# Performance work log

Measured on AMD Instinct MI355X. Metric: run time of the kernel, lower is better.

Reference implementation:

```python
import jax, jax.numpy as jnp
from jax import lax
import numpy as np

NS, NQ = 115, 23          # support / query node counts (1 node per graph here)
GS, GQ, C = 115, 23, 23   # support graphs (5-shot x 23-way), query graphs, classes
D = 1024


def _seg_mean(x, idx, n):
    # scatter-mean along axis 0 (matches torch_scatter reduce='mean'; empty segments -> 0)
    s = jax.ops.segment_sum(x, idx, num_segments=n)
    cnt = jax.ops.segment_sum(jnp.ones(x.shape[0], x.dtype), idx, num_segments=n)
    return s / jnp.maximum(cnt, 1.0).reshape((n,) + (1,) * (x.ndim - 1))


def _cnn(x, cw1, cb1, cw_rest, cb_rest):
    def block(h, w, b):
        h = lax.conv_general_dilated(h, w, (1, 1), 'SAME',
                                     dimension_numbers=('NCHW', 'OIHW', 'NCHW'))
        h = jax.nn.relu(h + b[None, :, None, None])
        return lax.reduce_window(h, -jnp.inf, lax.max, (1, 1, 2, 2), (1, 1, 2, 2), 'VALID')
    x = block(x, cw1, cb1)
    for i in range(cw_rest.shape[0]):
        x = block(x, cw_rest[i], cb_rest[i])
    return x.reshape(x.shape[0], -1)  # [N, 1024]


def _agg_mean(x, edge_index, n):
    # PyG propagate: message x_j = x[src], scatter-mean onto dst
    return _seg_mean(x[edge_index[0]], edge_index[1], n)


def setup_inputs() -> dict:
    key = jax.random.key(0)
    ks = jax.random.split(key, 12)
    s = 0.05
    return {
        'support_x': jax.random.normal(ks[0], (NS, 3, 256, 256), jnp.float32),
        'support_edge_index': jax.random.randint(ks[1], (2, 4096), 0, NS),
        'support_batch': jnp.arange(NS),          # 1 node per support graph
        'support_y': jnp.arange(GS) // 5,         # 5 graphs per class, classes 0..22
        'query_x': jax.random.normal(ks[2], (NQ, 3, 256, 256), jnp.float32),
        'query_edge_index': jax.random.randint(ks[3], (2, 1024), 0, NQ),
        'query_batch': jnp.arange(NQ),            # 1 node per query graph
        'query_y': jax.random.randint(ks[4], (GQ,), 0, C),
        'center': jax.random.normal(ks[5], (C, D), jnp.float32),
        'cw1': jax.random.normal(ks[6], (64, 3, 3, 3), jnp.float32) * s,
        'cb1': jnp.zeros((64,), jnp.float32),
        'cw_rest': jax.random.normal(ks[7], (5, 64, 64, 3, 3), jnp.float32) * s,
        'cb_rest': jnp.zeros((5, 64), jnp.float32),
        'lin2_w': jax.random.normal(ks[8], (D, D), jnp.float32) * 0.03,   # [in,out]
        'lin2_b': jnp.zeros((D,), jnp.float32),
        'mlp_w': jax.random.normal(ks[9], (2 * D, D), jnp.float32) * 0.02,  # [in,out]
        'mlp_b': jnp.zeros((D,), jnp.float32),
    }


def reference(support_x, support_edge_index, support_batch, support_y,
              query_x, query_edge_index, query_batch, query_y, center,
              cw1, cb1, cw_rest, cb_rest, lin2_w, lin2_b, mlp_w, mlp_b):
    n_cls = center.shape[0]

    def feats(x, ei):
        n = x.shape[0]
        h1 = _cnn(x, cw1, cb1, cw_rest, cb_rest)          # conv1 s_x1 = x (flatten feats)
        sx = _agg_mean(h1, ei, n) * h1                    # conv1 update: agg * x
        h2 = sx @ lin2_w + lin2_b                         # conv2 Linear(1024,1024)
        h2 = _agg_mean(h2, ei, n) * h2                    # conv2 update: agg * x
        return jnp.concatenate([h1, h2], axis=-1) @ mlp_w + mlp_b  # [N, 1024]

    s_x = feats(support_x, support_edge_index)            # [Ns, D]
    q_x = feats(query_x, query_edge_index)                # [Nq, D]
    gs = support_y.shape[0]
    gq = query_y.shape[0]

    # per-query-node RBF distances, scatter-mean over support graphs, log-softmax over D
    a = jnp.exp(-(s_x[None, :, :] - q_x[:, None, :]) ** 2)        # [Nq, Ns, D]
    a = _seg_mean(jnp.transpose(a, (1, 0, 2)), support_batch, gs) # [Gs, Nq, D]
    pd = jax.nn.log_softmax(jnp.transpose(a, (1, 0, 2)), axis=-1) # [Nq, Gs, D]

    s_xg = _seg_mean(s_x, support_batch, gs)              # [Gs, D]
    q_xg = _seg_mean(q_x, query_batch, gq)                # [Gq, D]
    pd = _seg_mean(pd, query_batch, gq)                   # [Gq, Gs, D]

    s_c = 0.25 * jnp.repeat(center, 5, axis=0) + 0.5 * s_xg       # [Gs, D]
    b = (jnp.exp(-(s_c[None, :, :] - q_xg[:, None, :]) ** 2) + pd).sum(-1)  # [Gq, Gs]
    b = jax.nn.log_softmax(b, axis=-1)
    dis = _seg_mean(b.T, support_y, n_cls).T              # [Gq, C]

    center_new = _seg_mean(s_xg, support_y, n_cls) * 0.5 + 0.25 * center

    y = jax.nn.one_hot(query_y, n_cls, dtype=jnp.float32)
    loss = -(y * jax.nn.log_softmax(dis, axis=-1)).sum()  # F.cross_entropy(soft, sum)
    acc = (jnp.argmax(dis, axis=1) == query_y).astype(jnp.float32).sum()
    return loss, acc, center_new
```

## Files before the change

### kernel.cpp

```cpp
#include <hip/hip_runtime.h>
#include <cstdint>
#include <cstddef>


typedef _Float16 f16x8 __attribute__((ext_vector_type(8)));
typedef __attribute__((ext_vector_type(4))) float f32x4;

#define WL 36864

__global__ __launch_bounds__(256)
void wtransform(const float* __restrict__ cwr, const float* __restrict__ cw1,
                _Float16* __restrict__ wbuf5, _Float16* __restrict__ w1buf) {
  int i = blockIdx.x * 256 + threadIdx.x;
  if (i < 184320) {
    int layer = i / 36864; int rem = i - layer * 36864;
    int tap = rem / 4096;  int r2 = rem - tap * 4096;
    int cc = r2 / 2048;    int r3 = r2 - cc * 2048;
    int nt = r3 / 512;     int r4 = r3 - nt * 512;
    int lane = r4 / 8;     int j = r4 - lane * 8;
    int ic = cc * 32 + (lane >> 4) * 8 + j;
    int oc = nt * 16 + (lane & 15);
    float w = cwr[(((size_t)layer * 64 + oc) * 64 + ic) * 9 + tap];
    wbuf5[(size_t)layer * 36864 + tap * 4096 + (cc * 4 + nt) * 512 + lane * 8 + j] =
        (_Float16)w;
  } else if (i < 184320 + 2048) {
    int e = i - 184320;
    int nt = e / 512; int r4 = e - nt * 512;
    int lane = r4 / 8; int j = r4 - lane * 8;
    int k = (lane >> 4) * 8 + j;
    float w = 0.f;
    if (k < 27) {
      int tap = k / 3, ic = k - tap * 3;
      int oc = nt * 16 + (lane & 15);
      w = cw1[((size_t)oc * 3 + ic) * 9 + tap];
    }
    w1buf[nt * 512 + lane * 8 + j] = (_Float16)w;
  }
}

__global__ __launch_bounds__(256)
void wtransform_lin(const float* __restrict__ w, _Float16* __restrict__ frag,
                    int KS) {
  int i = blockIdx.x * 256 + threadIdx.x;
  int total = KS * 64 * 512;
  if (i >= total) return;
  int ks = i / (64 * 512); int rem = i - ks * (64 * 512);
  int nt = rem / 512;      int r = rem - nt * 512;
  int lane = r / 8;        int j = r - lane * 8;
  int k = ks * 32 + (lane >> 4) * 8 + j;
  int n = nt * 16 + (lane & 15);
  frag[((size_t)ks * 64 + nt) * 512 + lane * 8 + j] = (_Float16)w[(size_t)k * 1024 + n];
}

template<int KTOT>
__global__ __launch_bounds__(256)
void gemm_mfma(const float* __restrict__ A1, const float* __restrict__ A2,
               const _Float16* __restrict__ frag,
               const float* __restrict__ bias, float* __restrict__ out, int M) {
  __shared__ f32x4 s_red[4][2][64];
  const int tid = threadIdx.x;
  const int wave = tid >> 6, lane = tid & 63;
  const int q = lane >> 4, ml = lane & 15;
  const int m0 = blockIdx.y * 16;
  const int nb = blockIdx.x;
  int row = m0 + ml; if (row >= M) row = M - 1;

  f32x4 acc[2];
#pragma unroll
  for (int nt = 0; nt < 2; ++nt) acc[nt] = (f32x4){0.f, 0.f, 0.f, 0.f};

  constexpr int KSW = KTOT / 128;
  const int ksBase = wave * KSW;
#pragma unroll 2
  for (int s = 0; s < KSW; ++s) {
    int ks = ksBase + s;
    int k0 = ks * 32 + q * 8;
    const float* ap;
    if constexpr (KTOT == 2048) {
      ap = (k0 >= 1024) ? (A2 + (size_t)row * 1024 + (k0 - 1024))
                        : (A1 + (size_t)row * 1024 + k0);
    } else {
      ap = A1 + (size_t)row * 1024 + k0;
    }
    float4 va = *(const float4*)ap;
    float4 vb = *(const float4*)(ap + 4);
    f16x8 av;
    av[0] = (_Float16)va.x; av[1] = (_Float16)va.y;
    av[2] = (_Float16)va.z; av[3] = (_Float16)va.w;
    av[4] = (_Float16)vb.x; av[5] = (_Float16)vb.y;
    av[6] = (_Float16)vb.z; av[7] = (_Float16)vb.w;
    const _Float16* fb = frag + ((size_t)ks * 64 + nb * 2) * 512 + lane * 8;
#pragma unroll
    for (int nt = 0; nt < 2; ++nt) {
      f16x8 bv = *(const f16x8*)(fb + nt * 512);
      acc[nt] = __builtin_amdgcn_mfma_f32_16x16x32_f16(av, bv, acc[nt], 0, 0, 0);
    }
  }
#pragma unroll
  for (int nt = 0; nt < 2; ++nt) s_red[wave][nt][lane] = acc[nt];
  __syncthreads();
  if (wave < 2) {
    int nt = wave;
    f32x4 sum = s_red[0][nt][lane];
#pragma unroll
    for (int w2 = 1; w2 < 4; ++w2) {
      f32x4 p = s_red[w2][nt][lane];
      sum[0] += p[0]; sum[1] += p[1]; sum[2] += p[2]; sum[3] += p[3];
    }
    int n = nb * 32 + nt * 16 + ml;
    float bv = bias[n];
#pragma unroll
    for (int r = 0; r < 4; ++r) {
      int m = m0 + q * 4 + r;
      if (m < M) out[(size_t)m * 1024 + n] = sum[r] + bv;
    }
  }
}

template<int TCX, int TCY, bool FP32OUT>
__global__ __launch_bounds__(256, 4)
void conv_mfma(const _Float16* __restrict__ act_in,
               void* __restrict__ act_out,
               const _Float16* __restrict__ wbuf,
               const float* __restrict__ bias,
               int IH, int IW) {
  constexpr int PX = TCX + 2, PY = TCY + 2;
  constexpr int MT = (TCX * TCY) / 64;
  __shared__ __align__(16) _Float16 s_patch[PY * PX * 40];

  const int tid = threadIdx.x;
  const int wave = tid >> 6, lane = tid & 63;
  const int q = lane >> 4, ml = lane & 15;
  const int x0 = blockIdx.x * TCX, y0 = blockIdx.y * TCY;
  const int img = blockIdx.z;

  f32x4 acc[MT][4];
#pragma unroll
  for (int mt = 0; mt < MT; ++mt)
#pragma unroll
    for (int nt = 0; nt < 4; ++nt)
      acc[mt][nt] = (f32x4){0.f, 0.f, 0.f, 0.f};

  int pxv[MT], pyv[MT];
#pragma unroll
  for (int mt = 0; mt < MT; ++mt) {
    int p = (wave * MT + mt) * 16 + ml;
    pxv[mt] = p % TCX;
    pyv[mt] = p / TCX;
  }

#pragma unroll 1
  for (int cc = 0; cc < 2; ++cc) {
    if (cc) __syncthreads();

    for (int u = tid; u < PY * PX * 4; u += 256) {
      int pos = u >> 2, sub = u & 3;
      int py = pos / PX, px = pos - py * PX;
      int gy = y0 - 1 + py, gx = x0 - 1 + px;
      uint4 v = {0u, 0u, 0u, 0u};
      if ((unsigned)gy < (unsigned)IH && (unsigned)gx < (unsigned)IW)
        v = *(const uint4*)(act_in +
              (((size_t)img * IH + gy) * IW + gx) * 64 + cc * 32 + sub * 8);
      *(uint4*)(s_patch + pos * 40 + sub * 8) = v;
    }

    const _Float16* wl = wbuf + cc * 2048 + lane * 8;
    f16x8 bw[4], bn[4];
#pragma unroll
    for (int f = 0; f < 4; ++f) bw[f] = *(const f16x8*)(wl + f * 512);

    __syncthreads();

#pragma unroll 1
    for (int tap = 0; tap < 9; ++tap) {
      if (tap < 8) {
        const _Float16* np = wl + (tap + 1) * 4096;
#pragma unroll
        for (int f = 0; f < 4; ++f) bn[f] = *(const f16x8*)(np + f * 512);
      }
      const int dy = tap / 3, dx = tap - dy * 3;
#pragma unroll
      for (int mt = 0; mt < MT; ++mt) {
        const _Float16* ap =
            s_patch + ((pyv[mt] + dy) * PX + (pxv[mt] + dx)) * 40 + q * 8;
        f16x8 av = *(const f16x8*)ap;
#pragma unroll
        for (int nt = 0; nt < 4; ++nt)
          acc[mt][nt] = __builtin_amdgcn_mfma_f32_16x16x32_f16(av, bw[nt],
                                                               acc[mt][nt], 0, 0, 0);
      }
#pragma unroll
      for (int f = 0; f < 4; ++f) bw[f] = bn[f];
    }
  }

  const int OH = IH >> 1, OW = IW >> 1;
#pragma unroll
  for (int nt = 0; nt < 4; ++nt) {
    int oc = nt * 16 + ml;
    float bvs = bias[oc];
    if constexpr (TCX == 16) {
#pragma unroll
      for (int mh = 0; mh < MT / 2; ++mh)
#pragma unroll
        for (int rh = 0; rh < 2; ++rh) {
          float a0 = fmaxf(acc[2 * mh][nt][2 * rh] + bvs, 0.f);
          float a1 = fmaxf(acc[2 * mh][nt][2 * rh + 1] + bvs, 0.f);
          float a2 = fmaxf(acc[2 * mh + 1][nt][2 * rh] + bvs, 0.f);
          float a3 = fmaxf(acc[2 * mh + 1][nt][2 * rh + 1] + bvs, 0.f);
          float m = fmaxf(fmaxf(a0, a1), fmaxf(a2, a3));
          int gy = (y0 >> 1) + wave * (MT / 2) + mh;
          int gx = (x0 >> 1) + q * 2 + rh;
          if (FP32OUT)
            ((float*)act_out)[(((size_t)img * 64 + oc) * OH + gy) * OW + gx] = m;
          else
            ((_Float16*)act_out)[(((size_t)img * OH + gy) * OW + gx) * 64 + oc] =
                (_Float16)m;
        }
    } else {
      float m01 = fmaxf(fmaxf(acc[0][nt][0] + bvs, 0.f), fmaxf(acc[0][nt][1] + bvs, 0.f));
      float m23 = fmaxf(fmaxf(acc[0][nt][2] + bvs, 0.f), fmaxf(acc[0][nt][3] + bvs, 0.f));
      float p0 = fmaxf(m01, __shfl_xor(m01, 32));
      float p1 = fmaxf(m23, __shfl_xor(m23, 32));
      if ((lane & 32) == 0) {
        int gy = (y0 >> 1) + wave;
        int gx0 = (x0 >> 1) + (q & 1) * 2;
        if (FP32OUT) {
          float* o = (float*)act_out + (((size_t)img * 64 + oc) * OH + gy) * OW + gx0;
          o[0] = p0; o[1] = p1;
        } else {
          _Float16* o = (_Float16*)act_out;
          o[(((size_t)img * OH + gy) * OW + gx0) * 64 + oc] = (_Float16)p0;
          o[(((size_t)img * OH + gy) * OW + gx0 + 1) * 64 + oc] = (_Float16)p1;
        }
      }
    }
  }
}

__global__ __launch_bounds__(256, 4)
void conv_l1(const float* __restrict__ in, _Float16* __restrict__ act_out,
             const _Float16* __restrict__ w1buf, const float* __restrict__ bias) {
  __shared__ __align__(16) _Float16 s_rawh[1280];

  const int tid = threadIdx.x;
  const int wave = tid >> 6, lane = tid & 63;
  const int q = lane >> 4, ml = lane & 15;
  const int x0 = blockIdx.x * 16, y0 = blockIdx.y * 16;
  const int img = blockIdx.z;

  if (tid < 308) s_rawh[972 + tid] = (_Float16)0.f;
  for (int i = tid; i < 972; i += 256) {
    int ic = i / 324, rem = i - ic * 324;
    int yy = rem / 18, xx = rem - yy * 18;
    int gy = y0 - 1 + yy, gx = x0 - 1 + xx;
    float v = 0.f;
    if ((unsigned)gy < 256u && (unsigned)gx < 256u)
      v = in[((size_t)img * 3 + ic) * 65536 + gy * 256 + gx];
    s_rawh[i] = (_Float16)v;
  }

  int offs[8];
#pragma unroll
  for (int j = 0; j < 8; ++j) {
    int k = q * 8 + j;
    int tap = k / 3, ic = k - tap * 3;
    int ddy = tap / 3, ddx = tap - ddy * 3;
    offs[j] = (k < 27) ? (ic * 324 + ddy * 18 + ddx + ml) : 972;
  }

  f16x8 bv[4];
#pragma unroll
  for (int nt = 0; nt < 4; ++nt)
    bv[nt] = *(const f16x8*)(w1buf + nt * 512 + lane * 8);

  __syncthreads();

  f32x4 acc[4][4];
#pragma unroll
  for (int t4 = 0; t4 < 4; ++t4)
#pragma unroll
    for (int nt = 0; nt < 4; ++nt)
      acc[t4][nt] = (f32x4){0.f, 0.f, 0.f, 0.f};

#pragma unroll
  for (int t4 = 0; t4 < 4; ++t4) {
    const int tb = (wave * 4 + t4) * 18;
    f16x8 av;
#pragma unroll
    for (int j = 0; j < 8; ++j) av[j] = s_rawh[offs[j] + tb];
#pragma unroll
    for (int nt = 0; nt < 4; ++nt)
      acc[t4][nt] = __builtin_amdgcn_mfma_f32_16x16x32_f16(av, bv[nt], acc[t4][nt], 0, 0, 0);
  }

#pragma unroll
  for (int nt = 0; nt < 4; ++nt) {
    int oc = nt * 16 + ml;
    float bvs = bias[oc];
#pragma unroll
    for (int mh = 0; mh < 2; ++mh)
#pragma unroll
      for (int rh = 0; rh < 2; ++rh) {
        float a0 = fmaxf(acc[2 * mh][nt][2 * rh] + bvs, 0.f);
        float a1 = fmaxf(acc[2 * mh][nt][2 * rh + 1] + bvs, 0.f);
        float a2 = fmaxf(acc[2 * mh + 1][nt][2 * rh] + bvs, 0.f);
        float a3 = fmaxf(acc[2 * mh + 1][nt][2 * rh + 1] + bvs, 0.f);
        float m = fmaxf(fmaxf(a0, a1), fmaxf(a2, a3));
        int gy = blockIdx.y * 8 + wave * 2 + mh;
        int gx = blockIdx.x * 8 + q * 2 + rh;
        act_out[(((size_t)img * 128 + gy) * 128 + gx) * 64 + oc] = (_Float16)m;
      }
  }
}

__global__ __launch_bounds__(256)
void edge_agg_mul(const float* __restrict__ h, const int* __restrict__ ei,
                  int E, float* __restrict__ out) {
  __shared__ int list[1024];
  __shared__ int cnt;
  const int n = blockIdx.x;
  const int tid = threadIdx.x;
  if (tid == 0) cnt = 0;
  __syncthreads();
  for (int e = tid; e < E; e += 256) {
    if (ei[E + e] == n) {
      int p = atomicAdd(&cnt, 1);
      list[p] = ei[e];
    }
  }
  __syncthreads();
  const int c = cnt;
  float ax = 0.f, ay = 0.f, az = 0.f, aw = 0.f;
#pragma unroll 4
  for (int i = 0; i < c; ++i) {
    const float4 v = ((const float4*)(h + (size_t)list[i] * 1024))[tid];
    ax += v.x; ay += v.y; az += v.z; aw += v.w;
  }
  float inv = 1.f / (float)(c > 0 ? c : 1);
  const float4 hv = ((const float4*)(h + (size_t)n * 1024))[tid];
  float4 o;
  o.x = ax * inv * hv.x; o.y = ay * inv * hv.y;
  o.z = az * inv * hv.z; o.w = aw * inv * hv.w;
  ((float4*)(out + (size_t)n * 1024))[tid] = o;
}

__global__ __launch_bounds__(256)
void rbf_pairs(const float* __restrict__ sx, const float* __restrict__ qx,
               const float* __restrict__ center, float* __restrict__ bpre) {
  int gid = blockIdx.x * 256 + threadIdx.x;
  int wid = gid >> 6;
  int lane = gid & 63;
  if (wid >= 23 * 115) return;
  int qq = wid / 115, s = wid - qq * 115;
  const float* sr = sx + (size_t)s * 1024;
  const float* qr = qx + (size_t)qq * 1024;
  const float* cr = center + (size_t)(s / 5) * 1024;
  float S1 = 0.f, S2 = 0.f, S3 = 0.f;
  for (int d = lane; d < 1024; d += 64) {
    float sv = sr[d], qv = qr[d];
    float df = sv - qv;
    float a = expf(-df * df);
    S1 += a;
    S2 += expf(a);
    float sc = 0.25f * cr[d] + 0.5f * sv;
    float d2 = sc - qv;
    S3 += expf(-d2 * d2);
  }
#pragma unroll
  for (int o = 32; o > 0; o >>= 1) {
    S1 += __shfl_down(S1, o);
    S2 += __shfl_down(S2, o);
    S3 += __shfl_down(S3, o);
  }
  if (lane == 0) bpre[wid] = S3 + S1 - 1024.f * logf(S2);
}

__global__ __launch_bounds__(256)
void center_new_k(const float* __restrict__ sx, const float* __restrict__ center,
                  const int* __restrict__ sy, float* __restrict__ out) {
  __shared__ int syv[115];
  int tid = threadIdx.x;
  if (tid < 115) syv[tid] = sy[tid];
  __syncthreads();
  int c = blockIdx.x;
  int d = blockIdx.y * 256 + tid;
  float sum = 0.f; int cnt = 0;
  for (int s = 0; s < 115; ++s)
    if (syv[s] == c) { sum += sx[(size_t)s * 1024 + d]; ++cnt; }
  out[2 + (size_t)c * 1024 + d] =
      0.5f * (sum / (float)(cnt > 0 ? cnt : 1)) + 0.25f * center[(size_t)c * 1024 + d];
}

__global__ __launch_bounds__(256)
void finalize_k(const float* __restrict__ bpre, const int* __restrict__ sy,
                const int* __restrict__ qy, float* __restrict__ out) {
  __shared__ float bls[23][115];
  __shared__ float dis[23][23];
  __shared__ int   syv[115];
  __shared__ float ccnt[23];
  __shared__ float lossq[23];
  __shared__ float accq[23];
  const int tid = threadIdx.x;
  if (tid < 115) syv[tid] = sy[tid];
  __syncthreads();
  if (tid < 23) {
    float mx = -3.4e38f;
    for (int s = 0; s < 115; ++s) mx = fmaxf(mx, bpre[tid * 115 + s]);
    float se = 0.f;
    for (int s = 0; s < 115; ++s) se += expf(bpre[tid * 115 + s] - mx);
    float lse = mx + logf(se);
    for (int s = 0; s < 115; ++s) bls[tid][s] = bpre[tid * 115 + s] - lse;
    int c = 0;
    for (int s = 0; s < 115; ++s) c += (syv[s] == tid);
    ccnt[tid] = (float)(c > 0 ? c : 1);
  }
  __syncthreads();
  for (int i = tid; i < 23 * 23; i += 256) {
    int qq = i / 23, c = i - qq * 23;
    float sum = 0.f;
    for (int s = 0; s < 115; ++s)
      if (syv[s] == c) sum += bls[qq][s];
    dis[qq][c] = sum / ccnt[c];
  }
  __syncthreads();
  if (tid < 23) {
    int qq = tid;
    float mx = -3.4e38f; int am = 0;
    for (int c = 0; c < 23; ++c) {
      float v = dis[qq][c];
      if (v > mx) { mx = v; am = c; }
    }
    float se = 0.f;
    for (int c = 0; c < 23; ++c) se += expf(dis[qq][c] - mx);
    float lse = mx + logf(se);
    int y = qy[qq];
    lossq[qq] = -(dis[qq][y] - lse);
    accq[qq] = (am == y) ? 1.f : 0.f;
  }
  __syncthreads();
  if (tid == 0) {
    float L = 0.f, A = 0.f;
    for (int qq = 0; qq < 23; ++qq) { L += lossq[qq]; A += accq[qq]; }
    out[0] = L;
    out[1] = A;
  }
}

extern "C" void kernel_launch(void* const* d_in, const int* in_sizes, int n_in,
                              void* d_out, int out_size, void* d_ws, size_t ws_size,
                              hipStream_t stream) {
  const float* sup_x  = (const float*)d_in[0];
  const int*   sup_ei = (const int*)d_in[1];
  const int*   sup_y  = (const int*)d_in[3];
  const float* q_x    = (const float*)d_in[4];
  const int*   q_ei   = (const int*)d_in[5];
  const int*   q_y    = (const int*)d_in[7];
  const float* center = (const float*)d_in[8];
  const float* cw1    = (const float*)d_in[9];
  const float* cb1    = (const float*)d_in[10];
  const float* cwr    = (const float*)d_in[11];
  const float* cbr    = (const float*)d_in[12];
  const float* l2w    = (const float*)d_in[13];
  const float* l2b    = (const float*)d_in[14];
  const float* mw     = (const float*)d_in[15];
  const float* mb     = (const float*)d_in[16];
  float* out = (float*)d_out;

  char* base = (char*)d_ws;
  size_t off = 0;
  auto alloc = [&](size_t n) { char* p = base + off; off += (n + 255) & ~(size_t)255; return p; };
  _Float16* wbuf5 = (_Float16*)alloc(5 * WL * 2);
  _Float16* w1buf = (_Float16*)alloc(2048 * 2);
  float* h1   = (float*)alloc(138 * 1024 * 4);
  float* sxb  = (float*)alloc(138 * 1024 * 4);
  float* h2p  = (float*)alloc(138 * 1024 * 4);
  float* h2   = (float*)alloc(138 * 1024 * 4);
  float* feat = (float*)alloc(138 * 1024 * 4);
  float* bpre = (float*)alloc(23 * 115 * 4);

  const size_t R1_FULL = 138ull * 64 * 64 * 64 * 2;
  const size_t R0_FULL = 115ull * 128 * 128 * 64 * 2;
  const size_t R0_23   = 23ull * 128 * 128 * 64 * 2;
  const size_t R1_SML  = 12ull * 64 * 64 * 64 * 2;
  const size_t R0_SML  = 12ull * 128 * 128 * 64 * 2;

  const int tier = (ws_size >= off + R1_FULL + R0_FULL + 4096) ? 0
                 : (ws_size >= off + R1_FULL + R0_23 + 4096)   ? 1 : 2;

  _Float16* region1 = (_Float16*)alloc(tier <= 1 ? R1_FULL : R1_SML);
  _Float16* region0 = (_Float16*)alloc(tier == 0 ? R0_FULL : (tier == 1 ? R0_23 : R0_SML));
  _Float16* l3out = region0;
  _Float16* l4out = region0 + (tier <= 1 ? 9043968u : 786432u);
  _Float16* l5out = region0 + (tier <= 1 ? 11304960u : 983040u);
  _Float16* wlin2 = region0;
  _Float16* wmlp  = region0 + 1048576u;

  wtransform<<<728, 256, 0, stream>>>(cwr, cw1, wbuf5, w1buf);

  if (tier == 0) {
    conv_l1<<<dim3(16, 16, 115), 256, 0, stream>>>(sup_x, region0, w1buf, cb1);
    conv_mfma<16, 16, false><<<dim3(8, 8, 115), 256, 0, stream>>>(
        region0, region1, wbuf5, cbr, 128, 128);
    conv_l1<<<dim3(16, 16, 23), 256, 0, stream>>>(q_x, region0, w1buf, cb1);
    conv_mfma<16, 16, false><<<dim3(8, 8, 23), 256, 0, stream>>>(
        region0, region1 + 115ull * 64 * 64 * 64, wbuf5, cbr, 128, 128);
    conv_mfma<16, 16, false><<<dim3(4, 4, 138), 256, 0, stream>>>(
        region1, l3out, wbuf5 + 1 * WL, cbr + 64, 64, 64);
    conv_mfma<16, 16, false><<<dim3(2, 2, 138), 256, 0, stream>>>(
        l3out, l4out, wbuf5 + 2 * WL, cbr + 128, 32, 32);
    conv_mfma<16, 16, false><<<dim3(1, 1, 138), 256, 0, stream>>>(
        l4out, l5out, wbuf5 + 3 * WL, cbr + 192, 16, 16);
    conv_mfma<8, 8, true><<<dim3(1, 1, 138), 256, 0, stream>>>(
        l5out, h1, wbuf5 + 4 * WL, cbr + 256, 8, 8);
  } else if (tier == 1) {
    for (int c = 0; c < 6; ++c) {
      const float* xin = (c < 5) ? (sup_x + (size_t)c * 23 * 3 * 65536) : q_x;
      conv_l1<<<dim3(16, 16, 23), 256, 0, stream>>>(xin, region0, w1buf, cb1);
      conv_mfma<16, 16, false><<<dim3(8, 8, 23), 256, 0, stream>>>(
          region0, region1 + (size_t)c * 23 * 64 * 64 * 64, wbuf5, cbr, 128, 128);
    }
    conv_mfma<16, 16, false><<<dim3(4, 4, 138), 256, 0, stream>>>(
        region1, l3out, wbuf5 + 1 * WL, cbr + 64, 64, 64);
    conv_mfma<16, 16, false><<<dim3(2, 2, 138), 256, 0, stream>>>(
        l3out, l4out, wbuf5 + 2 * WL, cbr + 128, 32, 32);
    conv_mfma<16, 16, false><<<dim3(1, 1, 138), 256, 0, stream>>>(
        l4out, l5out, wbuf5 + 3 * WL, cbr + 192, 16, 16);
    conv_mfma<8, 8, true><<<dim3(1, 1, 138), 256, 0, stream>>>(
        l5out, h1, wbuf5 + 4 * WL, cbr + 256, 8, 8);
  } else {
    auto run_chain = [&](const float* xin, int n, int gb) {
      conv_l1<<<dim3(16, 16, n), 256, 0, stream>>>(xin, region0, w1buf, cb1);
      conv_mfma<16, 16, false><<<dim3(8, 8, n), 256, 0, stream>>>(
          region0, region1, wbuf5, cbr, 128, 128);
      conv_mfma<16, 16, false><<<dim3(4, 4, n), 256, 0, stream>>>(
          region1, l3out, wbuf5 + 1 * WL, cbr + 64, 64, 64);
      conv_mfma<16, 16, false><<<dim3(2, 2, n), 256, 0, stream>>>(
          l3out, l4out, wbuf5 + 2 * WL, cbr + 128, 32, 32);
      conv_mfma<16, 16, false><<<dim3(1, 1, n), 256, 0, stream>>>(
          l4out, l5out, wbuf5 + 3 * WL, cbr + 192, 16, 16);
      conv_mfma<8, 8, true><<<dim3(1, 1, n), 256, 0, stream>>>(
          l5out, h1 + (size_t)gb * 1024, wbuf5 + 4 * WL, cbr + 256, 8, 8);
    };
    for (int i0 = 0; i0 < 115; i0 += 12)
      run_chain(sup_x + (size_t)i0 * 3 * 65536, (115 - i0 < 12) ? 115 - i0 : 12, i0);
    for (int i0 = 0; i0 < 23; i0 += 12)
      run_chain(q_x + (size_t)i0 * 3 * 65536, (23 - i0 < 12) ? 23 - i0 : 12, 115 + i0);
  }

  wtransform_lin<<<4096, 256, 0, stream>>>(l2w, wlin2, 32);
  wtransform_lin<<<8192, 256, 0, stream>>>(mw, wmlp, 64);

  edge_agg_mul<<<115, 256, 0, stream>>>(h1, sup_ei, 4096, sxb);
  edge_agg_mul<<<23, 256, 0, stream>>>(h1 + 115 * 1024, q_ei, 1024, sxb + 115 * 1024);
  gemm_mfma<1024><<<dim3(32, 9), 256, 0, stream>>>(sxb, nullptr, wlin2, l2b, h2p, 138);
  edge_agg_mul<<<115, 256, 0, stream>>>(h2p, sup_ei, 4096, h2);
  edge_agg_mul<<<23, 256, 0, stream>>>(h2p + 115 * 1024, q_ei, 1024, h2 + 115 * 1024);
  gemm_mfma<2048><<<dim3(32, 9), 256, 0, stream>>>(h1, h2, wmlp, mb, feat, 138);

  rbf_pairs<<<(23 * 115 * 64 + 255) / 256, 256, 0, stream>>>(
      feat, feat + 115 * 1024, center, bpre);
  center_new_k<<<dim3(23, 4), 256, 0, stream>>>(feat, center, sup_y, out);
  finalize_k<<<1, 256, 0, stream>>>(bpre, sup_y, q_y, out);
}
```

Measured before the change: 744.1 us.

## Add two-wave conv kernel with larger per-wave register tiles and weight prefetch

```diff
diff --git a/kernel.cpp b/kernel.cpp
--- a/kernel.cpp
+++ b/kernel.cpp
@@ -114,6 +114,99 @@
       int m = m0 + q * 4 + r;
       if (m < M) out[(size_t)m * 1024 + n] = sum[r] + bv;
     }
+  }
+}
+
+template<bool FP32OUT>
+__global__ __launch_bounds__(128, 2)
+void conv_mfma2(const _Float16* __restrict__ act_in,
+                void* __restrict__ act_out,
+                const _Float16* __restrict__ wbuf,
+                const float* __restrict__ bias,
+                int IH, int IW) {
+  constexpr int PX = 18, PY = 18;
+  __shared__ __align__(16) _Float16 s_patch[PY * PX * 40];
+
+  const int tid = threadIdx.x;
+  const int wave = tid >> 6, lane = tid & 63;
+  const int q = lane >> 4, ml = lane & 15;
+  const int x0 = blockIdx.x * 16, y0 = blockIdx.y * 16;
+  const int img = blockIdx.z;
+
+  f32x4 acc[8][4];
+#pragma unroll
+  for (int mt = 0; mt < 8; ++mt)
+#pragma unroll
+    for (int nt = 0; nt < 4; ++nt)
+      acc[mt][nt] = (f32x4){0.f, 0.f, 0.f, 0.f};
+
+#pragma unroll 1
+  for (int cc = 0; cc < 2; ++cc) {
+    if (cc) __syncthreads();
+
+    for (int u = tid; u < PY * PX * 4; u += 128) {
+      int pos = u >> 2, sub = u & 3;
+      int py = pos / PX, px = pos - py * PX;
+      int gy = y0 - 1 + py, gx = x0 - 1 + px;
+      uint4 v = {0u, 0u, 0u, 0u};
+      if ((unsigned)gy < (unsigned)IH && (unsigned)gx < (unsigned)IW)
+        v = *(const uint4*)(act_in +
+              (((size_t)img * IH + gy) * IW + gx) * 64 + cc * 32 + sub * 8);
+      *(uint4*)(s_patch + pos * 40 + sub * 8) = v;
+    }
+
+    const _Float16* wl = wbuf + cc * 2048 + lane * 8;
+    f16x8 bw[4], bn[4];
+#pragma unroll
+    for (int f = 0; f < 4; ++f) bw[f] = *(const f16x8*)(wl + f * 512);
+
+    __syncthreads();
+
+#pragma unroll 1
+    for (int tap = 0; tap < 9; ++tap) {
+      if (tap < 8) {
+        const _Float16* np = wl + (tap + 1) * 4096;
+#pragma unroll
+        for (int f = 0; f < 4; ++f) bn[f] = *(const f16x8*)(np + f * 512);
+      }
+      const int dy = tap / 3, dx = tap - dy * 3;
+#pragma unroll
+      for (int mt = 0; mt < 8; ++mt) {
+        const _Float16* ap =
+            s_patch + ((wave * 8 + mt + dy) * PX + (ml + dx)) * 40 + q * 8;
+        f16x8 av = *(const f16x8*)ap;
+#pragma unroll
+        for (int nt = 0; nt < 4; ++nt)
+          acc[mt][nt] = __builtin_amdgcn_mfma_f32_16x16x32_f16(av, bw[nt],
+                                                               acc[mt][nt], 0, 0, 0);
+      }
+#pragma unroll
+      for (int f = 0; f < 4; ++f) bw[f] = bn[f];
+    }
+  }
+
+  const int OH = IH >> 1, OW = IW >> 1;
+#pragma unroll
+  for (int nt = 0; nt < 4; ++nt) {
+    int oc = nt * 16 + ml;
+    float bvs = bias[oc];
+#pragma unroll
+    for (int mh = 0; mh < 4; ++mh)
+#pragma unroll
+      for (int rh = 0; rh < 2; ++rh) {
+        float a0 = fmaxf(acc[2 * mh][nt][2 * rh] + bvs, 0.f);
+        float a1 = fmaxf(acc[2 * mh][nt][2 * rh + 1] + bvs, 0.f);
+        float a2 = fmaxf(acc[2 * mh + 1][nt][2 * rh] + bvs, 0.f);
+        float a3 = fmaxf(acc[2 * mh + 1][nt][2 * rh + 1] + bvs, 0.f);
+        float m = fmaxf(fmaxf(a0, a1), fmaxf(a2, a3));
+        int gy = (y0 >> 1) + wave * 4 + mh;
+        int gx = (x0 >> 1) + q * 2 + rh;
+        if (FP32OUT)
+          ((float*)act_out)[(((size_t)img * 64 + oc) * OH + gy) * OW + gx] = m;
+        else
+          ((_Float16*)act_out)[(((size_t)img * OH + gy) * OW + gx) * 64 + oc] =
+              (_Float16)m;
+      }
   }
 }
 
@@ -500,16 +593,16 @@
 
   if (tier == 0) {
     conv_l1<<<dim3(16, 16, 115), 256, 0, stream>>>(sup_x, region0, w1buf, cb1);
-    conv_mfma<16, 16, false><<<dim3(8, 8, 115), 256, 0, stream>>>(
+    conv_mfma2<false><<<dim3(8, 8, 115), 128, 0, stream>>>(
         region0, region1, wbuf5, cbr, 128, 128);
     conv_l1<<<dim3(16, 16, 23), 256, 0, stream>>>(q_x, region0, w1buf, cb1);
-    conv_mfma<16, 16, false><<<dim3(8, 8, 23), 256, 0, stream>>>(
+    conv_mfma2<false><<<dim3(8, 8, 23), 128, 0, stream>>>(
         region0, region1 + 115ull * 64 * 64 * 64, wbuf5, cbr, 128, 128);
-    conv_mfma<16, 16, false><<<dim3(4, 4, 138), 256, 0, stream>>>(
+    conv_mfma2<false><<<dim3(4, 4, 138), 128, 0, stream>>>(
         region1, l3out, wbuf5 + 1 * WL, cbr + 64, 64, 64);
-    conv_mfma<16, 16, false><<<dim3(2, 2, 138), 256, 0, stream>>>(
+    conv_mfma2<false><<<dim3(2, 2, 138), 128, 0, stream>>>(
         l3out, l4out, wbuf5 + 2 * WL, cbr + 128, 32, 32);
-    conv_mfma<16, 16, false><<<dim3(1, 1, 138), 256, 0, stream>>>(
+    conv_mfma2<false><<<dim3(1, 1, 138), 128, 0, stream>>>(
         l4out, l5out, wbuf5 + 3 * WL, cbr + 192, 16, 16);
     conv_mfma<8, 8, true><<<dim3(1, 1, 138), 256, 0, stream>>>(
         l5out, h1, wbuf5 + 4 * WL, cbr + 256, 8, 8);
@@ -517,27 +610,27 @@
     for (int c = 0; c < 6; ++c) {
       const float* xin = (c < 5) ? (sup_x + (size_t)c * 23 * 3 * 65536) : q_x;
       conv_l1<<<dim3(16, 16, 23), 256, 0, stream>>>(xin, region0, w1buf, cb1);
-      conv_mfma<16, 16, false><<<dim3(8, 8, 23), 256, 0, stream>>>(
+      conv_mfma2<false><<<dim3(8, 8, 23), 128, 0, stream>>>(
           region0, region1 + (size_t)c * 23 * 64 * 64 * 64, wbuf5, cbr, 128, 128);
     }
-    conv_mfma<16, 16, false><<<dim3(4, 4, 138), 256, 0, stream>>>(
+    conv_mfma2<false><<<dim3(4, 4, 138), 128, 0, stream>>>(
         region1, l3out, wbuf5 + 1 * WL, cbr + 64, 64, 64);
-    conv_mfma<16, 16, false><<<dim3(2, 2, 138), 256, 0, stream>>>(
+    conv_mfma2<false><<<dim3(2, 2, 138), 128, 0, stream>>>(
         l3out, l4out, wbuf5 + 2 * WL, cbr + 128, 32, 32);
-    conv_mfma<16, 16, false><<<dim3(1, 1, 138), 256, 0, stream>>>(
+    conv_mfma2<false><<<dim3(1, 1, 138), 128, 0, stream>>>(
         l4out, l5out, wbuf5 + 3 * WL, cbr + 192, 16, 16);
     conv_mfma<8, 8, true><<<dim3(1, 1, 138), 256, 0, stream>>>(
         l5out, h1, wbuf5 + 4 * WL, cbr + 256, 8, 8);
   } else {
     auto run_chain = [&](const float* xin, int n, int gb) {
       conv_l1<<<dim3(16, 16, n), 256, 0, stream>>>(xin, region0, w1buf, cb1);
-      conv_mfma<16, 16, false><<<dim3(8, 8, n), 256, 0, stream>>>(
+      conv_mfma2<false><<<dim3(8, 8, n), 128, 0, stream>>>(
           region0, region1, wbuf5, cbr, 128, 128);
-      conv_mfma<16, 16, false><<<dim3(4, 4, n), 256, 0, stream>>>(
+      conv_mfma2<false><<<dim3(4, 4, n), 128, 0, stream>>>(
           region1, l3out, wbuf5 + 1 * WL, cbr + 64, 64, 64);
-      conv_mfma<16, 16, false><<<dim3(2, 2, n), 256, 0, stream>>>(
+      conv_mfma2<false><<<dim3(2, 2, n), 128, 0, stream>>>(
           l3out, l4out, wbuf5 + 2 * WL, cbr + 128, 32, 32);
-      conv_mfma<16, 16, false><<<dim3(1, 1, n), 256, 0, stream>>>(
+      conv_mfma2<false><<<dim3(1, 1, n), 128, 0, stream>>>(
           l4out, l5out, wbuf5 + 3 * WL, cbr + 192, 16, 16);
       conv_mfma<8, 8, true><<<dim3(1, 1, n), 256, 0, stream>>>(
           l5out, h1 + (size_t)gb * 1024, wbuf5 + 4 * WL, cbr + 256, 8, 8);
```

Result: slower. 816.4 us (+9.7%).
